# Kernel optimization log

Measured on AMD Instinct MI355X. Metric: run time of the kernel, lower is better.

The kernel has to match this reference:

```python
import jax, jax.numpy as jnp
import numpy as np

D_MODEL, D_K, D_V, NUM_HEADS = 1024, 64, 64, 16
B, T = 4, 2048


def setup_inputs() -> dict:
    key = jax.random.key(0)
    ks = jax.random.split(key, 9)
    s = 0.02
    inp = {
        "input_Q": jax.random.normal(ks[0], (B, T, D_MODEL), dtype=jnp.float32),
        # causal mask: True = masked out (matches torch masked_fill semantics)
        "mask": jnp.triu(jnp.ones((T, T), dtype=bool), k=1),
        "Wq": jax.random.normal(ks[1], (D_MODEL, D_K * NUM_HEADS), dtype=jnp.float32) * s,
        "bq": jnp.zeros((D_K * NUM_HEADS,), dtype=jnp.float32),
        "Wk": jax.random.normal(ks[2], (D_MODEL, D_K * NUM_HEADS), dtype=jnp.float32) * s,
        "bk": jnp.zeros((D_K * NUM_HEADS,), dtype=jnp.float32),
        "Wv": jax.random.normal(ks[3], (D_MODEL, D_V * NUM_HEADS), dtype=jnp.float32) * s,
        "bv": jnp.zeros((D_V * NUM_HEADS,), dtype=jnp.float32),
        "Wo": jax.random.normal(ks[4], (D_V * NUM_HEADS, D_MODEL), dtype=jnp.float32) * s,
        "bo": jnp.zeros((D_MODEL,), dtype=jnp.float32),
    }
    return inp


def reference(input_Q, mask, Wq, bq, Wk, bk, Wv, bv, Wo, bo):
    b, t, _ = input_Q.shape
    h, dk, dv = NUM_HEADS, D_K, D_V
    # projections, then split heads: [b, t, h*d] -> [b, h, t, d]
    Q = (input_Q @ Wq + bq).reshape(b, t, h, dk).transpose(0, 2, 1, 3)
    K = (input_Q @ Wk + bk).reshape(b, t, h, dk).transpose(0, 2, 1, 3)
    V = (input_Q @ Wv + bv).reshape(b, t, h, dv).transpose(0, 2, 1, 3)
    # scaled dot-product attention with full [b, h, t, t] scores (as original)
    scores = jnp.einsum("bhqd,bhkd->bhqk", Q, K) * (1.0 / np.sqrt(dk).astype(np.float32))
    scores = jnp.where(mask, jnp.float32(-jnp.inf), scores)
    attn = jax.nn.softmax(scores, axis=-1)
    ctx = jnp.einsum("bhqk,bhkd->bhqd", attn, V)  # [b, h, t, dv]
    combined = ctx.transpose(0, 2, 1, 3).reshape(b, t, h * dv)
    return combined @ Wo + bo
```

## Files before the change

kernel.cpp:

```cpp
#include <hip/hip_runtime.h>
#include <hip/hip_bf16.h>
#include <stdint.h>

#define B_  4
#define T_  2048
#define H_  16
#define DH  64
#define DM  1024

typedef unsigned short u16;
typedef float  f32x4  __attribute__((ext_vector_type(4)));
typedef u16    u16x4  __attribute__((ext_vector_type(4)));
typedef __bf16 bf16x8 __attribute__((ext_vector_type(8)));
typedef bf16x8 __attribute__((may_alias, aligned(16))) bf16x8_a;
typedef u16x4  __attribute__((may_alias, aligned(8)))  u16x4_a;
typedef f32x4  __attribute__((may_alias, aligned(16))) f32x4_a;

__device__ __forceinline__ void gld16(void* lds, const void* g) {
  __builtin_amdgcn_global_load_lds((const __attribute__((address_space(1))) unsigned int*)g,
                                   (__attribute__((address_space(3))) unsigned int*)lds,
                                   16, 0, 0);
}
__device__ __forceinline__ u16 f2b(float f) {
  __bf16 h = (__bf16)f; return __builtin_bit_cast(unsigned short, h);
}

__global__ void prep(const float* __restrict__ X,
                     const float* __restrict__ Wq, const float* __restrict__ Wk,
                     const float* __restrict__ Wv, const float* __restrict__ Wo,
                     u16* __restrict__ Xb,
                     u16* __restrict__ WqT, u16* __restrict__ WkT,
                     u16* __restrict__ WvT, u16* __restrict__ WoT) {
  if (blockIdx.z == 4) {
    const int bi = blockIdx.y * 16 + blockIdx.x;
#pragma unroll
    for (int p = 0; p < 32; ++p) {
      const int i = bi * 32768 + p * 1024 + threadIdx.x * 4;
      const f32x4 v = *(const f32x4*)&X[i];
      u16x4 o;
      o.x = f2b(v.x); o.y = f2b(v.y); o.z = f2b(v.z); o.w = f2b(v.w);
      *(u16x4_a*)&Xb[i] = o;
    }
    return;
  }
  const float* in; u16* out;
  switch (blockIdx.z) {
    case 0: in = Wq; out = WqT; break;
    case 1: in = Wk; out = WkT; break;
    case 2: in = Wv; out = WvT; break;
    default: in = Wo; out = WoT; break;
  }
  __shared__ u16 t[64][65];
  const int bx = blockIdx.x * 64, by = blockIdx.y * 64;
  const int tx = threadIdx.x & 63, ty = threadIdx.x >> 6;
  for (int i = ty; i < 64; i += 4) t[i][tx] = f2b(in[(size_t)(by + i) * DM + bx + tx]);
  __syncthreads();
  for (int i = ty; i < 64; i += 4) out[(size_t)(bx + i) * DM + by + tx] = t[tx][i];
}

__device__ __forceinline__ void gemm_bt_128(
    const u16* __restrict__ A, const u16* __restrict__ BT,
    const float* __restrict__ bias, float oscale,
    u16* __restrict__ C, float* __restrict__ Cf, int mode,
    int m0, int n0)
{
  constexpr int K = 1024, N = 1024;
  __shared__ __attribute__((aligned(16))) u16 lAB[128 * 128];
  u16* lA = lAB;
  u16* lB = lAB + 128 * 64;
  const int tid  = threadIdx.x;
  const int lane = tid & 63;
  const int quad = lane >> 4, ln = lane & 15;
  const int ln7 = ln & 7;
  const int wave = tid >> 6;
  const int wm = wave >> 1, wn = wave & 1;

  const f32x4 fz = {0.f, 0.f, 0.f, 0.f};
  f32x4 acc[4][4];
#pragma unroll
  for (int i = 0; i < 4; i++)
#pragma unroll
    for (int j = 0; j < 4; j++) acc[i][j] = fz;

  for (int k0 = 0; k0 < K; k0 += 64) {
    __syncthreads();
#pragma unroll
    for (int p = 0; p < 4; ++p) {
      const int P = p * 256 + tid;
      const int row = P >> 3, c = (P & 7) ^ (row & 7);
      gld16(&lA[P * 8], &A [(size_t)(m0 + row) * K + k0 + c * 8]);
      gld16(&lB[P * 8], &BT[(size_t)(n0 + row) * K + k0 + c * 8]);
    }
    __syncthreads();
#pragma unroll
    for (int ks = 0; ks < 2; ++ks) {
      bf16x8 af[4], bf[4];
#pragma unroll
      for (int i = 0; i < 4; i++)
        af[i] = *(const bf16x8_a*)&lA[(wm * 64 + i * 16 + ln) * 64 + (((ks * 4 + quad) ^ ln7) << 3)];
#pragma unroll
      for (int j = 0; j < 4; j++)
        bf[j] = *(const bf16x8_a*)&lB[(wn * 64 + j * 16 + ln) * 64 + (((ks * 4 + quad) ^ ln7) << 3)];
#pragma unroll
      for (int i = 0; i < 4; i++)
#pragma unroll
        for (int j = 0; j < 4; j++)
          acc[i][j] = __builtin_amdgcn_mfma_f32_16x16x32_bf16(af[i], bf[j], acc[i][j], 0, 0, 0);
    }
  }

  if (mode == 0) {
    __syncthreads();
#pragma unroll
    for (int j = 0; j < 4; j++) {
      const int nl = wn * 64 + j * 16 + ln;
      const float bn = bias[n0 + nl];
      const int cc = nl >> 3, wic = nl & 7;
#pragma unroll
      for (int i = 0; i < 4; i++) {
#pragma unroll
        for (int r = 0; r < 4; r++) {
          const int ml = wm * 64 + i * 16 + quad * 4 + r;
          lAB[ml * 128 + ((cc ^ ((ml >> 2) & 7)) << 3) + wic] =
              f2b((acc[i][j][r] + bn) * oscale);
        }
      }
    }
    __syncthreads();
    const int bb = m0 >> 11, t0 = m0 & 2047, h0 = n0 >> 6;
#pragma unroll
    for (int it = 0; it < 8; ++it) {
      const int P = it * 256 + tid;
      const int ml = P >> 4, cc = P & 15;
      const bf16x8 v = *(const bf16x8_a*)&lAB[ml * 128 + ((cc ^ ((ml >> 2) & 7)) << 3)];
      const int h = h0 + (cc >> 3), d = (cc & 7) * 8;
      *(bf16x8_a*)&C[((size_t)((bb * H_ + h) * T_ + t0 + ml)) * DH + d] = v;
    }
    return;
  }

  if (mode == 1) {
    __syncthreads();
#pragma unroll
    for (int j = 0; j < 4; j++) {
      const int nl = wn * 64 + j * 16 + ln;
      const float bn = bias[n0 + nl];
#pragma unroll
      for (int i = 0; i < 4; i++) {
        const int ml = wm * 64 + i * 16 + quad * 4;
        u16x4 o;
#pragma unroll
        for (int r = 0; r < 4; r++) o[r] = f2b((acc[i][j][r] + bn) * oscale);
        const int sc = (ml >> 3) ^ (nl & 15);
        *(u16x4_a*)&lAB[nl * 128 + sc * 8 + (ml & 7)] = o;
      }
    }
    __syncthreads();
    const int bb = m0 >> 11, t0 = m0 & 2047;
#pragma unroll
    for (int it = 0; it < 8; ++it) {
      const int P = it * 256 + tid;
      const int nl = P >> 4, c = P & 15;
      const bf16x8 v = *(const bf16x8_a*)&lAB[nl * 128 + ((c ^ (nl & 15)) << 3)];
      const int n = n0 + nl, h = n >> 6, d = n & 63;
      *(bf16x8_a*)&C[((size_t)((bb * H_ + h) * DH + d)) * T_ + t0 + c * 8] = v;
    }
    return;
  }

  float* lF = (float*)lAB;
  __syncthreads();
#pragma unroll
  for (int h2 = 0; h2 < 2; ++h2) {
#pragma unroll
    for (int ii = 0; ii < 2; ++ii) {
      const int i = h2 * 2 + ii;
#pragma unroll
      for (int j = 0; j < 4; j++) {
        const int nl = wn * 64 + j * 16 + ln;
        const float bn = bias[n0 + nl];
        const int cf = nl >> 2, wic = nl & 3;
#pragma unroll
        for (int r = 0; r < 4; r++) {
          const int lr = wm * 32 + ii * 16 + quad * 4 + r;
          lF[lr * 128 + ((cf ^ ((lr >> 2) & 7)) << 2) + wic] = acc[i][j][r] + bn;
        }
      }
    }
    __syncthreads();
#pragma unroll
    for (int it = 0; it < 8; ++it) {
      const int P = it * 256 + tid;
      const int lr = P >> 5, cf = P & 31;
      const f32x4 v = *(const f32x4_a*)&lF[lr * 128 + ((cf ^ ((lr >> 2) & 7)) << 2)];
      const int ml = (lr >> 5) * 64 + h2 * 32 + (lr & 31);
      *(f32x4_a*)&Cf[(size_t)(m0 + ml) * N + n0 + cf * 4] = v;
    }
    __syncthreads();
  }
}

__global__ __launch_bounds__(256, 2) void qkv_gemm(
    const u16* __restrict__ X,
    const u16* __restrict__ WqT, const u16* __restrict__ WkT, const u16* __restrict__ WvT,
    const float* __restrict__ bq, const float* __restrict__ bk, const float* __restrict__ bv,
    u16* __restrict__ Qo, u16* __restrict__ Ko, u16* __restrict__ Vto)
{
  const int raw = blockIdx.x;
  const int swz = (raw & 7) * 192 + (raw >> 3);
  const int z = swz >> 9, r2 = swz & 511;
  const int m0 = (r2 >> 3) * 128, n0 = (r2 & 7) * 128;
  const u16 *BT; const float* bias; u16* C; float sc; int mode;
  if (z == 0)      { BT = WqT; bias = bq; C = Qo;  sc = 0.1803368801111144f; mode = 0; }
  else if (z == 1) { BT = WkT; bias = bk; C = Ko;  sc = 1.0f;                mode = 0; }
  else             { BT = WvT; bias = bv; C = Vto; sc = 1.0f;                mode = 1; }
  gemm_bt_128(X, BT, bias, sc, C, nullptr, mode, m0, n0);
}

__global__ __launch_bounds__(256, 2) void out_gemm(
    const u16* __restrict__ ctx, const u16* __restrict__ WoT,
    const float* __restrict__ bo, float* __restrict__ out)
{
  const int raw = blockIdx.x;
  const int swz = (raw & 7) * 64 + (raw >> 3);
  const int m0 = (swz >> 3) * 128, n0 = (swz & 7) * 128;
  gemm_bt_128(ctx, WoT, bo, 1.0f, nullptr, out, 2, m0, n0);
}

__global__ __launch_bounds__(512, 4) void flash_attn(
    const u16* __restrict__ Q, const u16* __restrict__ Kg,
    const u16* __restrict__ Vt, u16* __restrict__ ctx)
{
  __shared__ __attribute__((aligned(16))) u16 lK[2][128 * 64];
  __shared__ __attribute__((aligned(16))) u16 lV[2][64 * 128];
  __shared__ __attribute__((aligned(16))) u16 lP[128 * 64];

  const int bh = blockIdx.x;
  const int b  = bh >> 4, h = bh & 15;
  const int qi = 15 - blockIdx.y;
  const int q0 = qi * 128;
  const int tid = threadIdx.x;
  const int lane = tid & 63, wave = tid >> 6;
  const int quad = lane >> 4, ln = lane & 15;
  const int ln7 = ln & 7, ln8 = ln >> 3;
  const int w16 = wave * 16;

  const u16* Qbh = Q  + (size_t)bh * T_ * DH;
  const u16* Kbh = Kg + (size_t)bh * T_ * DH;
  const u16* Vbh = Vt + (size_t)bh * DH * T_;

  auto stage_kv = [&](int kt, int bufw) {
    const int t0 = kt << 7;
    u16* dK = lK[bufw]; u16* dV = lV[bufw];
#pragma unroll
    for (int p = 0; p < 2; ++p) {
      const int P = p * 512 + tid;
      const int row = P >> 3, c = (P & 7) ^ (row & 7);
      gld16(&dK[P * 8], &Kbh[(size_t)(t0 + row) * DH + c * 8]);
    }
#pragma unroll
    for (int p = 0; p < 2; ++p) {
      const int P = p * 512 + tid;
      const int row = P >> 4, c = (P & 15) ^ (row & 15);
      gld16(&dV[P * 8], &Vbh[(size_t)row * T_ + t0 + c * 8]);
    }
  };

#pragma unroll
  for (int p = 0; p < 2; ++p) {
    const int P = p * 512 + tid;
    const int row = P >> 3, c = (P & 7) ^ (row & 7);
    gld16(&lP[P * 8], &Qbh[(size_t)(q0 + row) * DH + c * 8]);
  }
  stage_kv(0, 0);
  asm volatile("s_waitcnt vmcnt(4)" ::: "memory");
  __builtin_amdgcn_s_barrier();
  bf16x8 aq[2];
#pragma unroll
  for (int ks = 0; ks < 2; ++ks)
    aq[ks] = *(const bf16x8_a*)&lP[(w16 + ln) * 64 + (((ks * 4 + quad) ^ ln7) << 3)];

  bf16x8 ones;
#pragma unroll
  for (int i = 0; i < 8; i++) ones[i] = (__bf16)1.0f;

  const f32x4 fz = {0.f, 0.f, 0.f, 0.f};
  f32x4 accO[4];
  f32x4 accL;
#pragma unroll
  for (int j = 0; j < 4; j++) accO[j] = fz;
  accL = fz;

  auto compute_tile = [&](int kt, const u16* lKb, const u16* lVb, bool MASK) {
    const int t0 = kt * 128;
#pragma unroll
    for (int half = 0; half < 2; ++half) {
      f32x4 s[4];
#pragma unroll
      for (int jj = 0; jj < 4; jj++) s[jj] = fz;
      __builtin_amdgcn_s_setprio(1);
#pragma unroll
      for (int ks = 0; ks < 2; ++ks) {
        bf16x8 bk4[4];
#pragma unroll
        for (int jj = 0; jj < 4; jj++)
          bk4[jj] = *(const bf16x8_a*)&lKb[((half * 4 + jj) * 16 + ln) * 64 + (((ks * 4 + quad) ^ ln7) << 3)];
#pragma unroll
        for (int jj = 0; jj < 4; jj++)
          s[jj] = __builtin_amdgcn_mfma_f32_16x16x32_bf16(aq[ks], bk4[jj], s[jj], 0, 0, 0);
      }
      __builtin_amdgcn_s_setprio(0);

#pragma unroll
      for (int jj = 0; jj < 4; jj++)
#pragma unroll
        for (int r = 0; r < 4; r++) {
          float z = s[jj][r];
          if (MASK) {
            const int qrow = q0 + w16 + quad * 4 + r;
            if ((t0 + (half * 4 + jj) * 16 + ln) > qrow) z = -INFINITY;
          }
          s[jj][r] = __builtin_amdgcn_exp2f(z);
        }

#pragma unroll
      for (int jj = 0; jj < 4; jj++) {
        const int c = jj * 2 + ln8;
#pragma unroll
        for (int r = 0; r < 4; r++) {
          const int row = w16 + quad * 4 + r;
          lP[row * 64 + ((c ^ (row & 7)) << 3) + ln7] = f2b(s[jj][r]);
        }
      }

#pragma unroll
      for (int ks2 = 0; ks2 < 2; ++ks2) {
        const int ks = half * 2 + ks2;
        bf16x8 ap, bv4[4];
        ap = *(const bf16x8_a*)&lP[(w16 + ln) * 64 + (((ks2 * 4 + quad) ^ ln7) << 3)];
#pragma unroll
        for (int j2 = 0; j2 < 4; j2++)
          bv4[j2] = *(const bf16x8_a*)&lVb[(j2 * 16 + ln) * 128 + (((ks * 4 + quad) ^ ln) << 3)];
        __builtin_amdgcn_s_setprio(1);
        accL = __builtin_amdgcn_mfma_f32_16x16x32_bf16(ap, ones, accL, 0, 0, 0);
#pragma unroll
        for (int j2 = 0; j2 < 4; j2++)
          accO[j2] = __builtin_amdgcn_mfma_f32_16x16x32_bf16(ap, bv4[j2], accO[j2], 0, 0, 0);
        __builtin_amdgcn_s_setprio(0);
      }
    }
  };

  int buf = 0;
  for (int kt = 0; kt < qi; ++kt) {
    __builtin_amdgcn_s_barrier();
    stage_kv(kt + 1, buf ^ 1);
    asm volatile("s_waitcnt vmcnt(4)" ::: "memory");
    __builtin_amdgcn_s_barrier();
    compute_tile(kt, lK[buf], lV[buf], false);
    buf ^= 1;
  }
  __builtin_amdgcn_s_barrier();
  asm volatile("s_waitcnt vmcnt(0)" ::: "memory");
  __builtin_amdgcn_s_barrier();
  compute_tile(qi, lK[buf], lV[buf], true);

#pragma unroll
  for (int r = 0; r < 4; r++) {
    const int qrow = q0 + w16 + quad * 4 + r;
    const float inv = 1.0f / accL[r];
#pragma unroll
    for (int j2 = 0; j2 < 4; j2++) {
      const int d = j2 * 16 + ln;
      ctx[((size_t)(b * T_ + qrow)) * DM + h * DH + d] = f2b(accO[j2][r] * inv);
    }
  }
}

extern "C" void kernel_launch(void* const* d_in, const int* in_sizes, int n_in,
                              void* d_out, int out_size, void* d_ws, size_t ws_size,
                              hipStream_t stream) {
  (void)in_sizes; (void)n_in; (void)out_size; (void)ws_size;
  const float* X  = (const float*)d_in[0];
  const float* Wq = (const float*)d_in[2];
  const float* bq = (const float*)d_in[3];
  const float* Wk = (const float*)d_in[4];
  const float* bk = (const float*)d_in[5];
  const float* Wv = (const float*)d_in[6];
  const float* bv = (const float*)d_in[7];
  const float* Wo = (const float*)d_in[8];
  const float* bo = (const float*)d_in[9];
  float* out = (float*)d_out;

  char* ws = (char*)d_ws;
  u16* WqT = (u16*)(ws + (0ull  << 20));
  u16* WkT = (u16*)(ws + (2ull  << 20));
  u16* WvT = (u16*)(ws + (4ull  << 20));
  u16* WoT = (u16*)(ws + (6ull  << 20));
  u16* Xb  = (u16*)(ws + (8ull  << 20));
  u16* Qb  = (u16*)(ws + (24ull << 20));
  u16* Kb  = (u16*)(ws + (40ull << 20));
  u16* Vtb = (u16*)(ws + (72ull << 20));
  u16* ctx = (u16*)(ws + (88ull << 20));

  prep<<<dim3(16, 16, 5), 256, 0, stream>>>(X, Wq, Wk, Wv, Wo, Xb, WqT, WkT, WvT, WoT);
  qkv_gemm<<<dim3(1536), 256, 0, stream>>>(Xb, WqT, WkT, WvT, bq, bk, bv, Qb, Kb, Vtb);
  flash_attn<<<dim3(64, 16), 512, 0, stream>>>(Qb, Kb, Vtb, ctx);
  out_gemm<<<dim3(512), 256, 0, stream>>>(ctx, WoT, bo, out);
}
```

Measured before the change: 251.7 us.

## Keep attention probabilities in registers via transposed QK MFMA and permlane swaps

The QK^T MFMA now takes its operands in swapped order, so the score tile is computed transposed. Each lane can then pack its probabilities into bf16 pairs with v_cvt_pk_bf16_f32 and rearrange them across lanes with permlane32/permlane16 swaps into the A-operand layout for the PV MFMA. This removes the LDS round trip for P (scalar ds writes followed by a read-back) and the lP buffer, which lowers LDS footprint. Q is now loaded straight from global memory into registers instead of being staged through LDS. The risks are the correctness of the lane-permutation mapping and the extra VALU/permlane instructions.

```diff
diff --git a/kernel.cpp b/kernel.cpp
--- a/kernel.cpp
+++ b/kernel.cpp
@@ -9,8 +9,10 @@
 #define DM  1024
 
 typedef unsigned short u16;
+typedef unsigned int   u32;
 typedef float  f32x4  __attribute__((ext_vector_type(4)));
 typedef u16    u16x4  __attribute__((ext_vector_type(4)));
+typedef u32    u32x4  __attribute__((ext_vector_type(4)));
 typedef __bf16 bf16x8 __attribute__((ext_vector_type(8)));
 typedef bf16x8 __attribute__((may_alias, aligned(16))) bf16x8_a;
 typedef u16x4  __attribute__((may_alias, aligned(8)))  u16x4_a;
@@ -23,6 +25,11 @@
 }
 __device__ __forceinline__ u16 f2b(float f) {
   __bf16 h = (__bf16)f; return __builtin_bit_cast(unsigned short, h);
+}
+__device__ __forceinline__ u32 cvtpk(float lo, float hi) {
+  u32 r;
+  asm("v_cvt_pk_bf16_f32 %0, %1, %2" : "=v"(r) : "v"(lo), "v"(hi));
+  return r;
 }
 
 __global__ void prep(const float* __restrict__ X,
@@ -233,7 +240,6 @@
 {
   __shared__ __attribute__((aligned(16))) u16 lK[2][128 * 64];
   __shared__ __attribute__((aligned(16))) u16 lV[2][64 * 128];
-  __shared__ __attribute__((aligned(16))) u16 lP[128 * 64];
 
   const int bh = blockIdx.x;
   const int b  = bh >> 4, h = bh & 15;
@@ -242,7 +248,7 @@
   const int tid = threadIdx.x;
   const int lane = tid & 63, wave = tid >> 6;
   const int quad = lane >> 4, ln = lane & 15;
-  const int ln7 = ln & 7, ln8 = ln >> 3;
+  const int ln7 = ln & 7;
   const int w16 = wave * 16;
 
   const u16* Qbh = Q  + (size_t)bh * T_ * DH;
@@ -266,19 +272,11 @@
     }
   };
 
-#pragma unroll
-  for (int p = 0; p < 2; ++p) {
-    const int P = p * 512 + tid;
-    const int row = P >> 3, c = (P & 7) ^ (row & 7);
-    gld16(&lP[P * 8], &Qbh[(size_t)(q0 + row) * DH + c * 8]);
-  }
   stage_kv(0, 0);
-  asm volatile("s_waitcnt vmcnt(4)" ::: "memory");
-  __builtin_amdgcn_s_barrier();
+  const u16* qr = &Qbh[(size_t)(q0 + w16 + ln) * DH + quad * 8];
   bf16x8 aq[2];
-#pragma unroll
-  for (int ks = 0; ks < 2; ++ks)
-    aq[ks] = *(const bf16x8_a*)&lP[(w16 + ln) * 64 + (((ks * 4 + quad) ^ ln7) << 3)];
+  aq[0] = *(const bf16x8_a*)&qr[0];
+  aq[1] = *(const bf16x8_a*)&qr[32];
 
   bf16x8 ones;
 #pragma unroll
@@ -293,6 +291,7 @@
 
   auto compute_tile = [&](int kt, const u16* lKb, const u16* lVb, bool MASK) {
     const int t0 = kt * 128;
+    const int qrow_l = q0 + w16 + ln;
 #pragma unroll
     for (int half = 0; half < 2; ++half) {
       f32x4 s[4];
@@ -307,7 +306,7 @@
           bk4[jj] = *(const bf16x8_a*)&lKb[((half * 4 + jj) * 16 + ln) * 64 + (((ks * 4 + quad) ^ ln7) << 3)];
 #pragma unroll
         for (int jj = 0; jj < 4; jj++)
-          s[jj] = __builtin_amdgcn_mfma_f32_16x16x32_bf16(aq[ks], bk4[jj], s[jj], 0, 0, 0);
+          s[jj] = __builtin_amdgcn_mfma_f32_16x16x32_bf16(bk4[jj], aq[ks], s[jj], 0, 0, 0);
       }
       __builtin_amdgcn_s_setprio(0);
 
@@ -317,35 +316,39 @@
         for (int r = 0; r < 4; r++) {
           float z = s[jj][r];
           if (MASK) {
-            const int qrow = q0 + w16 + quad * 4 + r;
-            if ((t0 + (half * 4 + jj) * 16 + ln) > qrow) z = -INFINITY;
+            const int krow = t0 + (half * 4 + jj) * 16 + quad * 4 + r;
+            if (krow > qrow_l) z = -INFINITY;
           }
           s[jj][r] = __builtin_amdgcn_exp2f(z);
         }
 
-#pragma unroll
-      for (int jj = 0; jj < 4; jj++) {
-        const int c = jj * 2 + ln8;
-#pragma unroll
-        for (int r = 0; r < 4; r++) {
-          const int row = w16 + quad * 4 + r;
-          lP[row * 64 + ((c ^ (row & 7)) << 3) + ln7] = f2b(s[jj][r]);
-        }
-      }
-
-#pragma unroll
-      for (int ks2 = 0; ks2 < 2; ++ks2) {
-        const int ks = half * 2 + ks2;
-        bf16x8 ap, bv4[4];
-        ap = *(const bf16x8_a*)&lP[(w16 + ln) * 64 + (((ks2 * 4 + quad) ^ ln7) << 3)];
+      bf16x8 ap2[2];
+#pragma unroll
+      for (int g = 0; g < 2; ++g) {
+        u32 a = cvtpk(s[2 * g][0], s[2 * g][1]);
+        u32 bw = cvtpk(s[2 * g][2], s[2 * g][3]);
+        u32 c = cvtpk(s[2 * g + 1][0], s[2 * g + 1][1]);
+        u32 d = cvtpk(s[2 * g + 1][2], s[2 * g + 1][3]);
+        asm volatile("v_permlane32_swap_b32 %0, %1" : "+v"(a), "+v"(c));
+        asm volatile("v_permlane32_swap_b32 %0, %1" : "+v"(bw), "+v"(d));
+        asm volatile("v_permlane16_swap_b32 %0, %1" : "+v"(a), "+v"(c));
+        asm volatile("v_permlane16_swap_b32 %0, %1" : "+v"(bw), "+v"(d));
+        const u32x4 w = {a, bw, c, d};
+        ap2[g] = __builtin_bit_cast(bf16x8, w);
+      }
+
+#pragma unroll
+      for (int g = 0; g < 2; ++g) {
+        const int ks = half * 2 + g;
+        bf16x8 bv4[4];
 #pragma unroll
         for (int j2 = 0; j2 < 4; j2++)
           bv4[j2] = *(const bf16x8_a*)&lVb[(j2 * 16 + ln) * 128 + (((ks * 4 + quad) ^ ln) << 3)];
         __builtin_amdgcn_s_setprio(1);
-        accL = __builtin_amdgcn_mfma_f32_16x16x32_bf16(ap, ones, accL, 0, 0, 0);
+        accL = __builtin_amdgcn_mfma_f32_16x16x32_bf16(ap2[g], ones, accL, 0, 0, 0);
 #pragma unroll
         for (int j2 = 0; j2 < 4; j2++)
-          accO[j2] = __builtin_amdgcn_mfma_f32_16x16x32_bf16(ap, bv4[j2], accO[j2], 0, 0, 0);
+          accO[j2] = __builtin_amdgcn_mfma_f32_16x16x32_bf16(ap2[g], bv4[j2], accO[j2], 0, 0, 0);
         __builtin_amdgcn_s_setprio(0);
       }
     }
```

Result: faster. 239.2 us (-5.0%).
